# Kernel optimization log

Hardware: AMD Instinct MI355X
Metric: run time of the kernel (lower is better)

The kernel has to match this reference:

```python
import jax, jax.numpy as jnp
import numpy as np

VOCAB, D_MODEL, DICT, TOP_K = 50257, 512, 16384, 32
N_CONCEPTS, N_RELATIONS = 16, 6
B, S = 1024, 32


def sparse_topk(coeffs, top_k):
    # abs-topk along last dim, keep signed values, scatter to dense
    _, idx = jax.lax.top_k(jnp.abs(coeffs), top_k)          # [B, k]
    signed = jnp.take_along_axis(coeffs, idx, axis=-1)      # [B, k]
    rows = jnp.arange(coeffs.shape[0])[:, None]
    return jnp.zeros_like(coeffs).at[rows, idx].set(signed)


def setup_inputs() -> dict:
    key = jax.random.key(0)
    ks = jax.random.split(key, 16)
    f = lambda k, shape, scale: jax.random.normal(k, shape, dtype=jnp.float32) * scale
    inp = {
        'clean_tokens': jax.random.randint(ks[0], (B, S), 0, VOCAB),
        'noisy_tokens': jax.random.randint(ks[1], (B, S), 0, VOCAB),
        'embedding': f(ks[2], (VOCAB, D_MODEL), 1.0),
        'enc_w1': f(ks[3], (D_MODEL, D_MODEL), D_MODEL ** -0.5),
        'enc_b1': jnp.zeros((D_MODEL,), jnp.float32),
        'enc_w2': f(ks[4], (D_MODEL, D_MODEL), D_MODEL ** -0.5),
        'enc_b2': jnp.zeros((D_MODEL,), jnp.float32),
        'shared_atoms': f(ks[5], (DICT, D_MODEL), 0.04),
        'router_w': f(ks[6], (DICT, D_MODEL), D_MODEL ** -0.5),
        'concept_delta_w': f(ks[7], (DICT, D_MODEL), D_MODEL ** -0.5),
        'relation_delta_w': f(ks[8], (DICT, D_MODEL), D_MODEL ** -0.5),
        'concept_head_w': f(ks[9], (N_CONCEPTS, D_MODEL), D_MODEL ** -0.5),
        'concept_head_b': jnp.zeros((N_CONCEPTS,), jnp.float32),
        'relation_head_w': f(ks[10], (N_RELATIONS, D_MODEL), D_MODEL ** -0.5),
        'relation_head_b': jnp.zeros((N_RELATIONS,), jnp.float32),
    }
    return inp


def reference(clean_tokens, noisy_tokens, embedding, enc_w1, enc_b1, enc_w2, enc_b2,
              shared_atoms, router_w, concept_delta_w, relation_delta_w,
              concept_head_w, concept_head_b, relation_head_w, relation_head_b):
    def pooled(tokens):
        x = embedding[tokens].mean(axis=1)                       # [B, D]
        h = jax.nn.silu(x @ enc_w1.T + enc_b1)
        return h @ enc_w2.T + enc_b2

    def encode(p, delta_w):
        coeffs = p @ router_w.T + 0.3 * (p @ delta_w.T)          # [B, DICT]
        sparse = sparse_topk(coeffs, TOP_K)
        rep = sparse @ shared_atoms                              # [B, D]
        return rep, sparse

    clean_p = pooled(clean_tokens)
    noisy_p = pooled(noisy_tokens)
    c_rep, c_sp = encode(clean_p, concept_delta_w)
    r_rep, r_sp = encode(clean_p, relation_delta_w)
    nc_rep, nc_sp = encode(noisy_p, concept_delta_w)
    nr_rep, nr_sp = encode(noisy_p, relation_delta_w)

    fused_clean = 0.2 * clean_p + 0.9 * c_rep + 0.9 * r_rep
    fused_noisy = 0.2 * noisy_p + 0.9 * nc_rep + 0.9 * nr_rep

    return (fused_clean @ concept_head_w.T + concept_head_b,
            fused_clean @ relation_head_w.T + relation_head_b,
            fused_noisy @ concept_head_w.T + concept_head_b,
            fused_noisy @ relation_head_w.T + relation_head_b,
            c_sp, r_sp, nc_sp, nr_sp)
```

## Files before the change

### kernel.cpp

```cpp
#include <hip/hip_runtime.h>


typedef _Float16 f16x8 __attribute__((ext_vector_type(8)));
typedef _Float16 f16x4 __attribute__((ext_vector_type(4)));
typedef float f32x4 __attribute__((ext_vector_type(4)));

#define OUT_SPARSE 45056
#define SPARSE_PER 16777216

__global__ __launch_bounds__(128) void pool_kernel(
    const int* __restrict__ ct, const int* __restrict__ nt,
    const float* __restrict__ emb, double* __restrict__ xout)
{
    const int row = blockIdx.x, s = blockIdx.y;
    const int tid = threadIdx.x;
    __shared__ int tk[32];
    const int* t = (s ? nt : ct) + row * 32;
    if (tid < 32) tk[tid] = t[tid];
    __syncthreads();
    const int d = tid * 4;
    double a0 = 0, a1 = 0, a2 = 0, a3 = 0;
    for (int i = 0; i < 32; ++i) {
        const float4 v = *(const float4*)(emb + (size_t)tk[i] * 512 + d);
        a0 += (double)v.x; a1 += (double)v.y; a2 += (double)v.z; a3 += (double)v.w;
    }
    double* o = xout + ((size_t)s * 1024 + row) * 512 + d;
    o[0] = a0 * 0.03125; o[1] = a1 * 0.03125; o[2] = a2 * 0.03125; o[3] = a3 * 0.03125;
}

__global__ __launch_bounds__(256) void enc_gemm(
    const double* __restrict__ A, const float* __restrict__ W,
    const float* __restrict__ bias, double* __restrict__ C,
    _Float16* __restrict__ C16, int act)
{
    __shared__ double Ask[16][68];
    __shared__ double Wsk[16][68];
    const int tid = threadIdx.x;
    const int m0 = blockIdx.y * 64, n0 = blockIdx.x * 64;
    const int ty = tid >> 4, tx = tid & 15;
    const int r = tid >> 2, c4 = (tid & 3) * 4;
    double acc[4][4] = {};
    for (int k0 = 0; k0 < 512; k0 += 16) {
        const double4 av = *(const double4*)(A + (size_t)(m0 + r) * 512 + k0 + c4);
        const float4  wv = *(const float4*) (W + (size_t)(n0 + r) * 512 + k0 + c4);
        __syncthreads();
        Ask[c4 + 0][r] = av.x; Ask[c4 + 1][r] = av.y; Ask[c4 + 2][r] = av.z; Ask[c4 + 3][r] = av.w;
        Wsk[c4 + 0][r] = (double)wv.x; Wsk[c4 + 1][r] = (double)wv.y;
        Wsk[c4 + 2][r] = (double)wv.z; Wsk[c4 + 3][r] = (double)wv.w;
        __syncthreads();
#pragma unroll
        for (int k = 0; k < 16; ++k) {
            const double4 a = *(const double4*)&Ask[k][ty * 4];
            const double4 b = *(const double4*)&Wsk[k][tx * 4];
            const double aa[4] = {a.x, a.y, a.z, a.w};
            const double bb[4] = {b.x, b.y, b.z, b.w};
#pragma unroll
            for (int i = 0; i < 4; ++i)
#pragma unroll
                for (int j = 0; j < 4; ++j) acc[i][j] += aa[i] * bb[j];
        }
    }
#pragma unroll
    for (int i = 0; i < 4; ++i) {
        const int row = m0 + ty * 4 + i;
#pragma unroll
        for (int j = 0; j < 4; ++j) {
            const int col = n0 + tx * 4 + j;
            double v = acc[i][j] + (double)bias[col];
            if (act) v = v / (1.0 + exp(-v));
            C[(size_t)row * 512 + col] = v;
            if (C16) C16[(size_t)row * 512 + col] = (_Float16)v;
        }
    }
}

__global__ __launch_bounds__(256) void combine_kernel(
    const float* __restrict__ router, const float* __restrict__ cd,
    const float* __restrict__ rd, _Float16* __restrict__ wc,
    _Float16* __restrict__ wr)
{
    const size_t i = ((size_t)blockIdx.x * 256 + threadIdx.x) * 4;
    if (i >= (size_t)16384 * 512) return;
    const float4 r = *(const float4*)(router + i);
    const float4 c = *(const float4*)(cd + i);
    const float4 d = *(const float4*)(rd + i);
    f16x4 hc = { (_Float16)(r.x + 0.3f * c.x), (_Float16)(r.y + 0.3f * c.y),
                 (_Float16)(r.z + 0.3f * c.z), (_Float16)(r.w + 0.3f * c.w) };
    f16x4 hr = { (_Float16)(r.x + 0.3f * d.x), (_Float16)(r.y + 0.3f * d.y),
                 (_Float16)(r.z + 0.3f * d.z), (_Float16)(r.w + 0.3f * d.w) };
    *(f16x4*)(wc + i) = hc;
    *(f16x4*)(wr + i) = hr;
}

__global__ __launch_bounds__(256) void approx_gemm(
    const _Float16* __restrict__ P, const _Float16* __restrict__ Wc,
    const _Float16* __restrict__ Wr, float* __restrict__ outf)
{
    __shared__ _Float16 As[128 * 32];
    __shared__ _Float16 Bs[128 * 32];
    __shared__ _Float16 Cst[128 * 128];

    const int tid = threadIdx.x;
    const int q = blockIdx.z;
    const int n0 = blockIdx.x * 128, m0 = blockIdx.y * 128;
    const _Float16* A = P + (size_t)(q >> 1) * 524288;
    const _Float16* B = (q & 1) ? Wr : Wc;

    const int c0 = tid * 2, c1 = tid * 2 + 1;
    const int lane = tid & 63, w = tid >> 6;
    const int wm = w & 1, wn = w >> 1;
    const int lr = lane & 15, lk = lane >> 4;

    const f32x4 zero = {0.f, 0.f, 0.f, 0.f};
    f32x4 acc[4][4];
#pragma unroll
    for (int i = 0; i < 4; ++i)
#pragma unroll
        for (int j = 0; j < 4; ++j) acc[i][j] = zero;

    for (int kt = 0; kt < 16; ++kt) {
        const int k0 = kt * 32;
        const f16x8 a0v = *(const f16x8*)(A + (size_t)(m0 + (c0 >> 2)) * 512 + k0 + (c0 & 3) * 8);
        const f16x8 a1v = *(const f16x8*)(A + (size_t)(m0 + (c1 >> 2)) * 512 + k0 + (c1 & 3) * 8);
        const f16x8 b0v = *(const f16x8*)(B + (size_t)(n0 + (c0 >> 2)) * 512 + k0 + (c0 & 3) * 8);
        const f16x8 b1v = *(const f16x8*)(B + (size_t)(n0 + (c1 >> 2)) * 512 + k0 + (c1 & 3) * 8);
        __syncthreads();
        *(f16x8*)(As + c0 * 8) = a0v;
        *(f16x8*)(As + c1 * 8) = a1v;
        *(f16x8*)(Bs + c0 * 8) = b0v;
        *(f16x8*)(Bs + c1 * 8) = b1v;
        __syncthreads();
        f16x8 af[4], bf[4];
#pragma unroll
        for (int i = 0; i < 4; ++i) af[i] = *(const f16x8*)(As + (wm * 64 + i * 16 + lr) * 32 + lk * 8);
#pragma unroll
        for (int j = 0; j < 4; ++j) bf[j] = *(const f16x8*)(Bs + (wn * 64 + j * 16 + lr) * 32 + lk * 8);
#pragma unroll
        for (int i = 0; i < 4; ++i)
#pragma unroll
            for (int j = 0; j < 4; ++j)
                acc[i][j] = __builtin_amdgcn_mfma_f32_16x16x32_f16(af[i], bf[j], acc[i][j], 0, 0, 0);
    }
    __syncthreads();
#pragma unroll
    for (int i = 0; i < 4; ++i)
#pragma unroll
        for (int j = 0; j < 4; ++j)
#pragma unroll
            for (int rr = 0; rr < 4; ++rr)
                Cst[(wm * 64 + i * 16 + lk * 4 + rr) * 128 + (wn * 64 + j * 16 + lr)] =
                    (_Float16)acc[i][j][rr];
    __syncthreads();
    unsigned short* ob = (unsigned short*)outf + (size_t)2 * OUT_SPARSE + (size_t)q * 2 * SPARSE_PER;
#pragma unroll
    for (int p = 0; p < 8; ++p) {
        const int cc = p * 256 + tid;
        const int rl = cc >> 4;
        const int ch = (cc & 15) * 8;
        const float4 v = *(const float4*)(Cst + rl * 128 + ch);
        *(float4*)(ob + (size_t)(m0 + rl) * 32768 + n0 + ch) = v;
    }
}

__global__ __launch_bounds__(256) void select_kernel(
    const double* __restrict__ pw, const float* __restrict__ router,
    const float* __restrict__ cdelta, const float* __restrict__ rdelta,
    const float* __restrict__ atoms, float* __restrict__ outf,
    float* __restrict__ repw)
{
    constexpr int NCAP = 320, NRE = 64;
    const int row = blockIdx.x, q = blockIdx.y;
    const int pset = q >> 1;
    const int tid = threadIdx.x;

    __shared__ __align__(16) unsigned short rowv[16384];
    __shared__ unsigned hist[1024];
    __shared__ unsigned pscan[256];
    __shared__ double prow[512];
    __shared__ int cidx[NCAP];
    __shared__ unsigned short ckey[NCAP];
    __shared__ int r64i[NRE];
    __shared__ double cval[NRE];
    __shared__ float selv[32];
    __shared__ int seli[32];
    __shared__ int cnt, bstar;

    float* orow = outf + (size_t)OUT_SPARSE + (size_t)q * SPARSE_PER + (size_t)row * 16384;
    const double* prg = pw + ((size_t)pset * 1024 + row) * 512;

    for (int b = tid; b < 1024; b += 256) hist[b] = 0;
    if (tid == 0) { cnt = 0; bstar = -1; }
    prow[tid] = prg[tid];
    prow[tid + 256] = prg[tid + 256];
    __syncthreads();

    const uint4* arow = (const uint4*)orow;
    uint4* rv4 = (uint4*)rowv;
#pragma unroll
    for (int p = 0; p < 8; ++p) {
        const uint4 v = arow[p * 256 + tid];
        rv4[p * 256 + tid] = v;
        const unsigned uu[4] = {v.x, v.y, v.z, v.w};
#pragma unroll
        for (int e = 0; e < 4; ++e) {
            atomicAdd(&hist[(uu[e] & 0x7FFFu) >> 5], 1u);
            atomicAdd(&hist[((uu[e] >> 16) & 0x7FFFu) >> 5], 1u);
        }
    }
    __syncthreads();

    const float4 z4 = {0.f, 0.f, 0.f, 0.f};
    float4* o4 = (float4*)orow;
#pragma unroll
    for (int p = 0; p < 16; ++p) o4[p * 256 + tid] = z4;

    const unsigned h0 = hist[tid * 4], h1 = hist[tid * 4 + 1];
    const unsigned h2 = hist[tid * 4 + 2], h3 = hist[tid * 4 + 3];
    const unsigned l3 = h3, l2 = h2 + l3, l1 = h1 + l2, l0 = h0 + l1;
    pscan[tid] = l0;
    __syncthreads();
    for (int s = 1; s < 256; s <<= 1) {
        const unsigned v = (tid + s < 256) ? pscan[tid + s] : 0u;
        __syncthreads();
        pscan[tid] += v;
        __syncthreads();
    }
    {
        const unsigned above = (tid < 255) ? pscan[tid + 1] : 0u;
        int best = -1;
        if (l0 + above >= 64u) best = tid * 4;
        if (l1 + above >= 64u) best = tid * 4 + 1;
        if (l2 + above >= 64u) best = tid * 4 + 2;
        if (l3 + above >= 64u) best = tid * 4 + 3;
        if (best >= 0) atomicMax(&bstar, best);
    }
    __syncthreads();
    const unsigned kmin = (unsigned)(bstar < 0 ? 0 : bstar) << 5;

#pragma unroll
    for (int p = 0; p < 8; ++p) {
        const uint4 v = rv4[p * 256 + tid];
        const unsigned uu[4] = {v.x, v.y, v.z, v.w};
        const int base = (p * 256 + tid) * 8;
#pragma unroll
        for (int e = 0; e < 4; ++e) {
            const unsigned k0 = uu[e] & 0x7FFFu, k1 = (uu[e] >> 16) & 0x7FFFu;
            if (k0 >= kmin) { const int pos = atomicAdd(&cnt, 1); if (pos < NCAP) { cidx[pos] = base + e * 2;     ckey[pos] = (unsigned short)k0; } }
            if (k1 >= kmin) { const int pos = atomicAdd(&cnt, 1); if (pos < NCAP) { cidx[pos] = base + e * 2 + 1; ckey[pos] = (unsigned short)k1; } }
        }
    }
    __syncthreads();
    const int nc = min(cnt, NCAP);

    for (int p = tid; p < nc; p += 256) {
        const unsigned mk = ckey[p];
        const int mi = cidx[p];
        int rr = 0;
        for (int j = 0; j < nc; ++j) {
            const unsigned kj = ckey[j];
            rr += (kj > mk || (kj == mk && cidx[j] < mi)) ? 1 : 0;
        }
        if (rr < NRE) r64i[rr] = mi;
    }
    __syncthreads();

    const float* drow = (q & 1) ? rdelta : cdelta;
    const int w = tid >> 6, lane = tid & 63;
    for (int c = w; c < NRE; c += 4) {
        const int idx = r64i[c];
        const float4* rp4 = (const float4*)(router + (size_t)idx * 512);
        const float4* dp4 = (const float4*)(drow + (size_t)idx * 512);
        const float4 r0 = rp4[lane * 2], r1 = rp4[lane * 2 + 1];
        const float4 d0 = dp4[lane * 2], d1 = dp4[lane * 2 + 1];
        const double* pv = prow + lane * 8;
        double aR = pv[0] * (double)r0.x + pv[1] * (double)r0.y + pv[2] * (double)r0.z + pv[3] * (double)r0.w
                  + pv[4] * (double)r1.x + pv[5] * (double)r1.y + pv[6] * (double)r1.z + pv[7] * (double)r1.w;
        double aD = pv[0] * (double)d0.x + pv[1] * (double)d0.y + pv[2] * (double)d0.z + pv[3] * (double)d0.w
                  + pv[4] * (double)d1.x + pv[5] * (double)d1.y + pv[6] * (double)d1.z + pv[7] * (double)d1.w;
        for (int sh = 32; sh > 0; sh >>= 1) { aR += __shfl_down(aR, sh); aD += __shfl_down(aD, sh); }
        if (lane == 0) cval[c] = aR + 0.3 * aD;
    }
    __syncthreads();

    if (tid < NRE) {
        const double av = fabs(cval[tid]);
        const int mi = r64i[tid];
        int rr = 0;
        for (int j = 0; j < NRE; ++j) {
            const double aj = fabs(cval[j]);
            rr += (aj > av || (aj == av && r64i[j] < mi)) ? 1 : 0;
        }
        if (rr < 32) {
            const float fv = (float)cval[tid];
            selv[rr] = fv; seli[rr] = mi;
            orow[mi] = fv;
        }
    }
    __syncthreads();

    double a0 = 0, a1 = 0;
    for (int k = 0; k < 32; ++k) {
        const double v = (double)selv[k];
        const float* ar = atoms + (size_t)seli[k] * 512;
        a0 += v * (double)ar[tid];
        a1 += v * (double)ar[tid + 256];
    }
    float* rp = repw + ((size_t)q * 1024 + row) * 512;
    rp[tid] = (float)a0;
    rp[tid + 256] = (float)a1;
}

__global__ __launch_bounds__(256) void heads_kernel(
    const double* __restrict__ pw, const float* __restrict__ repw,
    const float* __restrict__ chw, const float* __restrict__ chb,
    const float* __restrict__ rhw, const float* __restrict__ rhb,
    float* __restrict__ out)
{
    const int row = blockIdx.x, s = blockIdx.y;
    const int tid = threadIdx.x;
    __shared__ double fused[512];
    const double* pr = pw + ((size_t)s * 1024 + row) * 512;
    const float* rc = repw + ((size_t)(s * 2 + 0) * 1024 + row) * 512;
    const float* rr = repw + ((size_t)(s * 2 + 1) * 1024 + row) * 512;
    for (int d = tid; d < 512; d += 256)
        fused[d] = 0.2 * pr[d] + 0.9 * (double)rc[d] + 0.9 * (double)rr[d];
    __syncthreads();
    const int w = tid >> 6, lane = tid & 63;
    for (int o = w; o < 22; o += 4) {
        const float* hw = (o < 16) ? (chw + (size_t)o * 512) : (rhw + (size_t)(o - 16) * 512);
        double acc = 0;
#pragma unroll
        for (int j = 0; j < 8; ++j) acc += fused[lane + 64 * j] * (double)hw[lane + 64 * j];
        for (int sh = 32; sh > 0; sh >>= 1) acc += __shfl_down(acc, sh);
        if (lane == 0) {
            if (o < 16) out[(s ? 22528 : 0) + row * 16 + o] = (float)(acc + (double)chb[o]);
            else        out[(s ? 38912 : 16384) + row * 6 + (o - 16)] = (float)(acc + (double)rhb[o - 16]);
        }
    }
}

extern "C" void kernel_launch(void* const* d_in, const int* in_sizes, int n_in,
                              void* d_out, int out_size, void* d_ws, size_t ws_size,
                              hipStream_t stream)
{
    const int*   ctok   = (const int*)d_in[0];
    const int*   ntok   = (const int*)d_in[1];
    const float* emb    = (const float*)d_in[2];
    const float* w1     = (const float*)d_in[3];
    const float* b1     = (const float*)d_in[4];
    const float* w2     = (const float*)d_in[5];
    const float* b2     = (const float*)d_in[6];
    const float* atoms  = (const float*)d_in[7];
    const float* router = (const float*)d_in[8];
    const float* cdelta = (const float*)d_in[9];
    const float* rdelta = (const float*)d_in[10];
    const float* chw    = (const float*)d_in[11];
    const float* chb    = (const float*)d_in[12];
    const float* rhw    = (const float*)d_in[13];
    const float* rhb    = (const float*)d_in[14];
    float* out = (float*)d_out;

    double*    xw   = (double*)d_ws;
    double*    hw   = xw + 1048576;
    double*    pw   = hw + 1048576;
    float*     repw = (float*)(pw + 1048576);
    _Float16*  pf16 = (_Float16*)(repw + 2097152);
    _Float16*  wcw  = pf16 + 1048576;
    _Float16*  wrw  = wcw + 8388608;

    pool_kernel<<<dim3(1024, 2), 128, 0, stream>>>(ctok, ntok, emb, xw);
    enc_gemm<<<dim3(8, 32), 256, 0, stream>>>(xw, w1, b1, hw, (_Float16*)nullptr, 1);
    enc_gemm<<<dim3(8, 32), 256, 0, stream>>>(hw, w2, b2, pw, pf16, 0);
    combine_kernel<<<8192, 256, 0, stream>>>(router, cdelta, rdelta, wcw, wrw);
    approx_gemm<<<dim3(128, 8, 4), 256, 0, stream>>>(pf16, wcw, wrw, out);
    select_kernel<<<dim3(1024, 4), 256, 0, stream>>>(pw, router, cdelta, rdelta, atoms, out, repw);
    heads_kernel<<<dim3(1024, 2), 256, 0, stream>>>(pw, repw, chw, chb, rhw, rhb, out);
}
```

Baseline: 924.5 us.

## Use async global-to-LDS loads in GEMM and prefilter select histogram by sigma

```diff
diff --git a/kernel.cpp b/kernel.cpp
--- a/kernel.cpp
+++ b/kernel.cpp
@@ -7,6 +7,15 @@
 
 #define OUT_SPARSE 45056
 #define SPARSE_PER 16777216
+
+#define ASYNC16(gp, lp) __builtin_amdgcn_global_load_lds(                      \
+    (const __attribute__((address_space(1))) void*)(gp),                       \
+    (__attribute__((address_space(3))) void*)(lp), 16, 0, 0)
+
+__device__ inline float h2f(unsigned s) {
+    _Float16 h = __builtin_bit_cast(_Float16, (unsigned short)(s & 0xFFFFu));
+    return (float)h;
+}
 
 __global__ __launch_bounds__(128) void pool_kernel(
     const int* __restrict__ ct, const int* __restrict__ nt,
@@ -106,11 +115,21 @@
     const _Float16* A = P + (size_t)(q >> 1) * 524288;
     const _Float16* B = (q & 1) ? Wr : Wc;
 
-    const int c0 = tid * 2, c1 = tid * 2 + 1;
     const int lane = tid & 63, w = tid >> 6;
     const int wm = w & 1, wn = w >> 1;
     const int lr = lane & 15, lk = lane >> 4;
 
+    const int ch0 = w * 2, ch1 = w * 2 + 1;
+    const int lrow = lane >> 2, lh = (lane & 3) * 8;
+    const _Float16* Ag0 = A + (size_t)(m0 + ch0 * 16 + lrow) * 512 + lh;
+    const _Float16* Ag1 = A + (size_t)(m0 + ch1 * 16 + lrow) * 512 + lh;
+    const _Float16* Bg0 = B + (size_t)(n0 + ch0 * 16 + lrow) * 512 + lh;
+    const _Float16* Bg1 = B + (size_t)(n0 + ch1 * 16 + lrow) * 512 + lh;
+    _Float16* Al0 = As + ch0 * 512;
+    _Float16* Al1 = As + ch1 * 512;
+    _Float16* Bl0 = Bs + ch0 * 512;
+    _Float16* Bl1 = Bs + ch1 * 512;
+
     const f32x4 zero = {0.f, 0.f, 0.f, 0.f};
     f32x4 acc[4][4];
 #pragma unroll
@@ -120,15 +139,11 @@
 
     for (int kt = 0; kt < 16; ++kt) {
         const int k0 = kt * 32;
-        const f16x8 a0v = *(const f16x8*)(A + (size_t)(m0 + (c0 >> 2)) * 512 + k0 + (c0 & 3) * 8);
-        const f16x8 a1v = *(const f16x8*)(A + (size_t)(m0 + (c1 >> 2)) * 512 + k0 + (c1 & 3) * 8);
-        const f16x8 b0v = *(const f16x8*)(B + (size_t)(n0 + (c0 >> 2)) * 512 + k0 + (c0 & 3) * 8);
-        const f16x8 b1v = *(const f16x8*)(B + (size_t)(n0 + (c1 >> 2)) * 512 + k0 + (c1 & 3) * 8);
-        __syncthreads();
-        *(f16x8*)(As + c0 * 8) = a0v;
-        *(f16x8*)(As + c1 * 8) = a1v;
-        *(f16x8*)(Bs + c0 * 8) = b0v;
-        *(f16x8*)(Bs + c1 * 8) = b1v;
+        __syncthreads();
+        ASYNC16(Ag0 + k0, Al0);
+        ASYNC16(Ag1 + k0, Al1);
+        ASYNC16(Bg0 + k0, Bl0);
+        ASYNC16(Bg1 + k0, Bl1);
         __syncthreads();
         f16x8 af[4], bf[4];
 #pragma unroll
@@ -156,9 +171,9 @@
     for (int p = 0; p < 8; ++p) {
         const int cc = p * 256 + tid;
         const int rl = cc >> 4;
-        const int ch = (cc & 15) * 8;
-        const float4 v = *(const float4*)(Cst + rl * 128 + ch);
-        *(float4*)(ob + (size_t)(m0 + rl) * 32768 + n0 + ch) = v;
+        const int chh = (cc & 15) * 8;
+        const float4 v = *(const float4*)(Cst + rl * 128 + chh);
+        *(float4*)(ob + (size_t)(m0 + rl) * 32768 + n0 + chh) = v;
     }
 }
 
@@ -168,12 +183,11 @@
     const float* __restrict__ atoms, float* __restrict__ outf,
     float* __restrict__ repw)
 {
-    constexpr int NCAP = 320, NRE = 64;
+    constexpr int NCAP = 160, NRE = 64;
     const int row = blockIdx.x, q = blockIdx.y;
     const int pset = q >> 1;
     const int tid = threadIdx.x;
 
-    __shared__ __align__(16) unsigned short rowv[16384];
     __shared__ unsigned hist[1024];
     __shared__ unsigned pscan[256];
     __shared__ double prow[512];
@@ -183,7 +197,9 @@
     __shared__ double cval[NRE];
     __shared__ float selv[32];
     __shared__ int seli[32];
+    __shared__ float wred[4];
     __shared__ int cnt, bstar;
+    __shared__ unsigned cutk_s;
 
     float* orow = outf + (size_t)OUT_SPARSE + (size_t)q * SPARSE_PER + (size_t)row * 16384;
     const double* prg = pw + ((size_t)pset * 1024 + row) * 512;
@@ -192,19 +208,43 @@
     if (tid == 0) { cnt = 0; bstar = -1; }
     prow[tid] = prg[tid];
     prow[tid + 256] = prg[tid + 256];
-    __syncthreads();
-
-    const uint4* arow = (const uint4*)orow;
-    uint4* rv4 = (uint4*)rowv;
+
+    uint4 rv[8];
+    const uint4* ar4 = (const uint4*)orow;
+#pragma unroll
+    for (int p = 0; p < 8; ++p) rv[p] = ar4[p * 256 + tid];
+
+    float ss = 0.f;
 #pragma unroll
     for (int p = 0; p < 8; ++p) {
-        const uint4 v = arow[p * 256 + tid];
-        rv4[p * 256 + tid] = v;
-        const unsigned uu[4] = {v.x, v.y, v.z, v.w};
+        const unsigned uu[4] = {rv[p].x, rv[p].y, rv[p].z, rv[p].w};
 #pragma unroll
         for (int e = 0; e < 4; ++e) {
-            atomicAdd(&hist[(uu[e] & 0x7FFFu) >> 5], 1u);
-            atomicAdd(&hist[((uu[e] >> 16) & 0x7FFFu) >> 5], 1u);
+            const float f0 = h2f(uu[e]), f1 = h2f(uu[e] >> 16);
+            ss = fmaf(f0, f0, ss);
+            ss = fmaf(f1, f1, ss);
+        }
+    }
+    for (int sh = 32; sh > 0; sh >>= 1) ss += __shfl_down(ss, sh);
+    const int w = tid >> 6, lane = tid & 63;
+    if (lane == 0) wred[w] = ss;
+    __syncthreads();
+    if (tid == 0) {
+        const float sig = sqrtf((wred[0] + wred[1] + wred[2] + wred[3]) * (1.f / 16384.f));
+        const _Float16 h = (_Float16)(2.0f * sig);
+        cutk_s = (unsigned)__builtin_bit_cast(unsigned short, h) & 0x7FFFu;
+    }
+    __syncthreads();
+    const unsigned cutk = cutk_s;
+
+#pragma unroll
+    for (int p = 0; p < 8; ++p) {
+        const unsigned uu[4] = {rv[p].x, rv[p].y, rv[p].z, rv[p].w};
+#pragma unroll
+        for (int e = 0; e < 4; ++e) {
+            const unsigned k0 = uu[e] & 0x7FFFu, k1 = (uu[e] >> 16) & 0x7FFFu;
+            if (k0 >= cutk) atomicAdd(&hist[k0 >> 5], 1u);
+            if (k1 >= cutk) atomicAdd(&hist[k1 >> 5], 1u);
         }
     }
     __syncthreads();
@@ -239,8 +279,7 @@
 
 #pragma unroll
     for (int p = 0; p < 8; ++p) {
-        const uint4 v = rv4[p * 256 + tid];
-        const unsigned uu[4] = {v.x, v.y, v.z, v.w};
+        const unsigned uu[4] = {rv[p].x, rv[p].y, rv[p].z, rv[p].w};
         const int base = (p * 256 + tid) * 8;
 #pragma unroll
         for (int e = 0; e < 4; ++e) {
@@ -265,7 +304,6 @@
     __syncthreads();
 
     const float* drow = (q & 1) ? rdelta : cdelta;
-    const int w = tid >> 6, lane = tid & 63;
     for (int c = w; c < NRE; c += 4) {
         const int idx = r64i[c];
         const float4* rp4 = (const float4*)(router + (size_t)idx * 512);
```

Result: faster. 868.4 us (-6.1%).
